# Kernel tuning notes

Measured on AMD Instinct MI355X. Metric: run time of the kernel, lower is better.

The kernel has to match this reference:

```python
import jax, jax.numpy as jnp
import numpy as np

N = 10000  # num_source_nodes == num_target_nodes

def setup_inputs() -> dict:
    key = jax.random.key(0)
    k1, k2 = jax.random.split(key)
    A_hat = jax.random.normal(k1, (N, N), dtype=jnp.float32)
    alpha = jax.random.uniform(k2, (N,), dtype=jnp.float32)
    return {"A_hat": A_hat, "alpha": alpha}

def reference(A_hat, alpha):
    # Original: A_new = (alpha_col * (A_hat * alpha_col).T).T
    # which equals A_new[i, j] = alpha[i] * alpha[j] * A_hat[i, j].
    # The scipy COO round-trip only repackages this dense result as sparse;
    # the underlying math is the symmetric diagonal rescaling below.
    return alpha[:, None] * A_hat * alpha[None, :]
```

## Files before the change

kernel.cpp:

```cpp
#include <hip/hip_runtime.h>
#include <hip/hip_bf16.h>


__global__ __launch_bounds__(256) void stable_factor_kernel(
    const float* __restrict__ A,
    const float* __restrict__ alpha,
    float* __restrict__ out,
    int N) {
    const int nvec = N >> 2;
    const int col4 = blockIdx.x * blockDim.x + threadIdx.x;
    const int row  = blockIdx.y;
    if (col4 >= nvec) return;

    const float ai = alpha[row];
    const size_t row_off = (size_t)row * (size_t)N;

    const float4* __restrict__ A4  = reinterpret_cast<const float4*>(A + row_off);
    const float4* __restrict__ al4 = reinterpret_cast<const float4*>(alpha);
    float4* __restrict__ O4        = reinterpret_cast<float4*>(out + row_off);

    float4 a = A4[col4];
    float4 b = al4[col4];

    float4 o;
    o.x = ai * b.x * a.x;
    o.y = ai * b.y * a.y;
    o.z = ai * b.z * a.z;
    o.w = ai * b.w * a.w;

    O4[col4] = o;
}

extern "C" void kernel_launch(void* const* d_in, const int* in_sizes, int n_in,
                              void* d_out, int out_size, void* d_ws, size_t ws_size,
                              hipStream_t stream) {
    const float* A     = (const float*)d_in[0];
    const float* alpha = (const float*)d_in[1];
    float* out         = (float*)d_out;

    const int N = in_sizes[1];
    const int nvec = N >> 2;

    dim3 block(256, 1, 1);
    dim3 grid((nvec + 255) / 256, N, 1);
    stable_factor_kernel<<<grid, block, 0, stream>>>(A, alpha, out, N);
}
```

Before: 146.4 us.

## Use persistent row-strided grid with nontemporal loads and stores

Replaces the 2D grid (one block per row chunk) with a fixed grid of 2048 blocks that loop over rows, each thread striding across columns. The streaming A loads and output stores now use nontemporal builtins so they bypass cache retention, leaving the reused alpha vector resident. A scalar tail loop is added for N not divisible by 4. The risks are fewer blocks in flight to hide memory latency, and different cache behaviour for a purely bandwidth-bound 800 MB stream.

Result: slower. 166.5 us (+13.8%).

```diff
diff --git a/kernel.cpp b/kernel.cpp
--- a/kernel.cpp
+++ b/kernel.cpp
@@ -1,34 +1,34 @@
 #include <hip/hip_runtime.h>
 #include <hip/hip_bf16.h>
 
+
+typedef float f32x4 __attribute__((ext_vector_type(4)));
 
 __global__ __launch_bounds__(256) void stable_factor_kernel(
     const float* __restrict__ A,
     const float* __restrict__ alpha,
     float* __restrict__ out,
-    int N) {
-    const int nvec = N >> 2;
-    const int col4 = blockIdx.x * blockDim.x + threadIdx.x;
-    const int row  = blockIdx.y;
-    if (col4 >= nvec) return;
+    int N, int nvec) {
 
-    const float ai = alpha[row];
-    const size_t row_off = (size_t)row * (size_t)N;
+    const f32x4* __restrict__ al4 = reinterpret_cast<const f32x4*>(alpha);
 
-    const float4* __restrict__ A4  = reinterpret_cast<const float4*>(A + row_off);
-    const float4* __restrict__ al4 = reinterpret_cast<const float4*>(alpha);
-    float4* __restrict__ O4        = reinterpret_cast<float4*>(out + row_off);
+    for (int row = blockIdx.x; row < N; row += gridDim.x) {
+        const float ai = alpha[row];
+        const size_t off = (size_t)row * (size_t)N;
+        const f32x4* __restrict__ A4 = reinterpret_cast<const f32x4*>(A + off);
+        f32x4* __restrict__ O4       = reinterpret_cast<f32x4*>(out + off);
 
-    float4 a = A4[col4];
-    float4 b = al4[col4];
+        for (int c = threadIdx.x; c < nvec; c += blockDim.x) {
+            f32x4 a = __builtin_nontemporal_load(&A4[c]);
+            f32x4 b = al4[c];
+            f32x4 o = (ai * b) * a;
+            __builtin_nontemporal_store(o, &O4[c]);
+        }
 
-    float4 o;
-    o.x = ai * b.x * a.x;
-    o.y = ai * b.y * a.y;
-    o.z = ai * b.z * a.z;
-    o.w = ai * b.w * a.w;
-
-    O4[col4] = o;
+        for (int j = (nvec << 2) + threadIdx.x; j < N; j += blockDim.x) {
+            out[off + j] = ai * alpha[j] * A[off + j];
+        }
+    }
 }
 
 extern "C" void kernel_launch(void* const* d_in, const int* in_sizes, int n_in,
@@ -38,10 +38,10 @@
     const float* alpha = (const float*)d_in[1];
     float* out         = (float*)d_out;
 
-    const int N = in_sizes[1];
+    const int N    = in_sizes[1];
     const int nvec = N >> 2;
 
     dim3 block(256, 1, 1);
-    dim3 grid((nvec + 255) / 256, N, 1);
-    stable_factor_kernel<<<grid, block, 0, stream>>>(A, alpha, out, N);
+    dim3 grid(2048, 1, 1);
+    stable_factor_kernel<<<grid, block, 0, stream>>>(A, alpha, out, N, nvec);
 }
```
